# Optimization experiments

Measured on AMD Instinct MI355X. Metric: run time of the kernel, lower is better.

The kernel has to match this reference:

```python
import jax, jax.numpy as jnp
import numpy as np

KERNEL_MUL = 2.0
KERNEL_NUM = 5


def _mmd(source, target):
    n = source.shape[0]
    m = target.shape[0]
    total = jnp.concatenate([source, target], axis=0)  # [n+m, d]
    sq = jnp.sum(total * total, axis=1)  # [n+m]
    l2 = sq[:, None] + sq[None, :] - 2.0 * (total @ total.T)  # [n+m, n+m]
    l2 = jnp.maximum(l2, 0.0)
    n_samples = n + m
    bandwidth = jnp.sum(l2) / (n_samples * n_samples - n_samples)
    bandwidth = bandwidth / (KERNEL_MUL ** (KERNEL_NUM // 2))
    # sum of KERNEL_NUM Gaussian kernels with geometric bandwidths
    kernels = sum(jnp.exp(-l2 / (bandwidth * KERNEL_MUL ** i)) for i in range(KERNEL_NUM))
    b = n  # batch_size = n, as in the torch code
    xx = jnp.sum(kernels[:b, :b]) / (n * n)
    yy = jnp.sum(kernels[b:, b:]) / (m * m)
    xy = jnp.sum(kernels[:b, b:]) / (n * m)
    yx = jnp.sum(kernels[b:, :b]) / (m * n)
    return xx + yy - xy - yx


def setup_inputs() -> dict:
    key = jax.random.key(0)
    k1, k2 = jax.random.split(key)
    source = jax.random.normal(k1, (4096, 256), dtype=jnp.float32)
    target = jax.random.normal(k2, (4096, 256), dtype=jnp.float32)
    return {"source": source, "target": target}


def reference(source, target):
    return _mmd(source, target)
```

## Files before the change

kernel.cpp:

```cpp
#include <hip/hip_runtime.h>
#include <hip/hip_bf16.h>

#define WS_SLOT_OFF   0
#define WS_NEGG_OFF   16640
#define WS_SQPART_OFF 16648
#define WS_CSPART_OFF 17672
#define WS_SQ_OFF     148744
#define WS_G_OFF      181520

#define NROW 8192
#define HALF 4096
#define DIM  256
#define TILE 128
#define NB   64
#define NBLK (NB * (NB + 1) / 2)
#define KC   32
#define NC   (DIM / KC)
#define BUFE (TILE * KC)
#define PREPB 128

typedef short  short8 __attribute__((ext_vector_type(8)));
typedef float  f32x4  __attribute__((ext_vector_type(4)));
typedef float  f32x2  __attribute__((ext_vector_type(2)));
typedef unsigned short us4 __attribute__((ext_vector_type(4)));

static __device__ __forceinline__ unsigned short f2bfbits(float f) {
    __hip_bfloat16 h = __float2bfloat16(f);
    return *reinterpret_cast<unsigned short*>(&h);
}
static __device__ __forceinline__ float bfbits2f(unsigned short u) {
    return __uint_as_float(((unsigned int)u) << 16);
}
static __device__ __forceinline__ void gl_lds16(const void* g, void* l) {
    __builtin_amdgcn_global_load_lds(
        (const __attribute__((address_space(1))) void*)g,
        (__attribute__((address_space(3))) void*)l, 16, 0, 0);
}

__global__ __launch_bounds__(256) void k_prep(const float* __restrict__ src,
                                              const float* __restrict__ tgt,
                                              unsigned short* __restrict__ G,
                                              float* __restrict__ sq,
                                              float* __restrict__ cspart,
                                              double* __restrict__ sqpart) {
    __shared__ float cs_lds[4 * 256];
    __shared__ double sq_lds[4];

    int t = threadIdx.x, wid = t >> 6, lane = t & 63;
    int r0 = blockIdx.x * 64;
    int c4 = lane * 4;

    float cs0 = 0.f, cs1 = 0.f, cs2 = 0.f, cs3 = 0.f;
    double wsq = 0.0;
    for (int i = 0; i < 16; ++i) {
        int row = r0 + wid + i * 4;
        const float* base = (row < HALF) ? (src + (size_t)row * DIM)
                                         : (tgt + (size_t)(row - HALF) * DIM);
        float4 v = *(const float4*)(base + c4);
        unsigned short u0 = f2bfbits(v.x), u1 = f2bfbits(v.y),
                       u2 = f2bfbits(v.z), u3 = f2bfbits(v.w);
        us4 uu = {u0, u1, u2, u3};
        *(us4*)(G + (size_t)row * DIM + c4) = uu;
        float r0f = bfbits2f(u0), r1f = bfbits2f(u1),
              r2f = bfbits2f(u2), r3f = bfbits2f(u3);
        cs0 += r0f; cs1 += r1f; cs2 += r2f; cs3 += r3f;
        float s = r0f * r0f + r1f * r1f + r2f * r2f + r3f * r3f;
        #pragma unroll
        for (int off = 32; off; off >>= 1) s += __shfl_down(s, off);
        if (lane == 0) { sq[row] = s; wsq += (double)s; }
    }
    cs_lds[wid * 256 + c4 + 0] = cs0;
    cs_lds[wid * 256 + c4 + 1] = cs1;
    cs_lds[wid * 256 + c4 + 2] = cs2;
    cs_lds[wid * 256 + c4 + 3] = cs3;
    if (lane == 0) sq_lds[wid] = wsq;
    __syncthreads();
    float s = cs_lds[t] + cs_lds[256 + t] + cs_lds[512 + t] + cs_lds[768 + t];
    cspart[blockIdx.x * 256 + t] = s;
    if (t == 0)
        sqpart[blockIdx.x] = sq_lds[0] + sq_lds[1] + sq_lds[2] + sq_lds[3];
}

__global__ __launch_bounds__(256) void k_bw(const float* __restrict__ cspart,
                                            const double* __restrict__ sqpart,
                                            double* __restrict__ negg) {
    __shared__ double red[256];
    __shared__ double red2[256];
    int t = threadIdx.x;
    double c = 0.0;
    for (int b = 0; b < PREPB; ++b) c += (double)cspart[b * 256 + t];
    double s = (t < PREPB) ? sqpart[t] : 0.0;
    red[t]  = s;
    red2[t] = c * c;
    __syncthreads();
    for (int off = 128; off; off >>= 1) {
        if (t < off) { red[t] += red[t + off]; red2[t] += red2[t + off]; }
        __syncthreads();
    }
    if (t == 0) {
        const double N = (double)NROW;
        double sum_l2 = 2.0 * N * red[0] - 2.0 * red2[0];
        double bw = sum_l2 / (N * N - N);
        bw = bw / 4.0;
        negg[0] = -1.4426950408889634 / (16.0 * bw);
    }
}

__global__ __launch_bounds__(256, 3) void k_mmd(const unsigned short* __restrict__ G,
                                                const float* __restrict__ sq,
                                                const double* __restrict__ negg,
                                                double* __restrict__ slots) {
    __shared__ unsigned short As[3 * BUFE];
    __shared__ unsigned short Bs[3 * BUFE];
    __shared__ double wsum[4];

    int bi = 0, rem = blockIdx.x;
    while (rem >= NB - bi) { rem -= NB - bi; ++bi; }
    int bj = bi + rem;

    int t = threadIdx.x, wid = t >> 6, lane = t & 63;
    int wr = wid >> 1, wc = wid & 1;
    int rl = lane & 15, klane = lane >> 4;

    const unsigned short* Abase = G + (size_t)bi * TILE * DIM;
    const unsigned short* Bbase = G + (size_t)bj * TILE * DIM;

    int lr0 = wid * 32 + (lane >> 2);
    int slog0 = (lane & 3) ^ ((lr0 >> 1) & 3);
    int lr1 = lr0 + 16;
    int slog1 = (lane & 3) ^ ((lr1 >> 1) & 3);
    size_t ga0 = (size_t)lr0 * DIM + slog0 * 8;
    size_t ga1 = (size_t)lr1 * DIM + slog1 * 8;
    int ld0 = (wid * 32) * KC;
    int ld1 = (wid * 32 + 16) * KC;

    int aoff[4], boff[4];
    #pragma unroll
    for (int f = 0; f < 4; ++f) {
        int ra = wr * 64 + f * 16 + rl;
        aoff[f] = ra * KC + ((klane ^ ((ra >> 1) & 3)) * 8);
        int rb = wc * 64 + f * 16 + rl;
        boff[f] = rb * KC + ((klane ^ ((rb >> 1) & 3)) * 8);
    }

    const f32x4 zero4 = {0.f, 0.f, 0.f, 0.f};
    f32x4 acc[4][4];
    #pragma unroll
    for (int i = 0; i < 4; ++i)
        #pragma unroll
        for (int j = 0; j < 4; ++j) acc[i][j] = zero4;

    #define STAGE(kc, b)                                                     \
        do {                                                                 \
            gl_lds16(Abase + ga0 + (kc) * KC, &As[(b) * BUFE + ld0]);        \
            gl_lds16(Bbase + ga0 + (kc) * KC, &Bs[(b) * BUFE + ld0]);        \
            gl_lds16(Abase + ga1 + (kc) * KC, &As[(b) * BUFE + ld1]);        \
            gl_lds16(Bbase + ga1 + (kc) * KC, &Bs[(b) * BUFE + ld1]);        \
        } while (0)

    STAGE(0, 0);
    STAGE(1, 1);

    #pragma unroll
    for (int kc = 0; kc < NC; ++kc) {
        if (kc < NC - 1) { asm volatile("s_waitcnt vmcnt(4)" ::: "memory"); }
        else             { asm volatile("s_waitcnt vmcnt(0)" ::: "memory"); }
        __builtin_amdgcn_s_barrier();
        __builtin_amdgcn_sched_barrier(0);
        if (kc + 2 < NC) STAGE(kc + 2, (kc + 2) % 3);

        const unsigned short* Ab = &As[(kc % 3) * BUFE];
        const unsigned short* Bb = &Bs[(kc % 3) * BUFE];
        short8 af[4], bfv[4];
        #pragma unroll
        for (int f = 0; f < 4; ++f) {
            af[f]  = *(const short8*)&Ab[aoff[f]];
            bfv[f] = *(const short8*)&Bb[boff[f]];
        }
        #pragma unroll
        for (int i = 0; i < 4; ++i)
            #pragma unroll
            for (int j = 0; j < 4; ++j)
                acc[i][j] = __builtin_amdgcn_mfma_f32_16x16x32_bf16(
                    af[i], bfv[j], acc[i][j], 0, 0, 0);
    }
    #undef STAGE

    int gi0 = bi * TILE + wr * 64;
    int gj0 = bj * TILE + wc * 64;
    float ng2 = (float)negg[0];
    float m2g = -2.0f * ng2;
    f32x2 m2g2 = {m2g, m2g};
    int rgrp = lane >> 4;

    float sqb4[4];
    #pragma unroll
    for (int j = 0; j < 4; ++j) sqb4[j] = sq[gj0 + j * 16 + rl] * ng2;

    f32x2 tsv = {0.f, 0.f};
    #pragma unroll
    for (int i = 0; i < 4; ++i) {
        int base = gi0 + i * 16 + rgrp * 4;
        f32x2 sa01 = {sq[base + 0] * ng2, sq[base + 1] * ng2};
        f32x2 sa23 = {sq[base + 2] * ng2, sq[base + 3] * ng2};
        #pragma unroll
        for (int j = 0; j < 4; ++j) {
            f32x2 sb = {sqb4[j], sqb4[j]};
            f32x2 x01 = {acc[i][j][0], acc[i][j][1]};
            f32x2 x23 = {acc[i][j][2], acc[i][j][3]};
            x01 = x01 * m2g2 + (sa01 + sb);
            x23 = x23 * m2g2 + (sa23 + sb);
            f32x2 e01, e23;
            e01.x = exp2f(x01.x); e01.y = exp2f(x01.y);
            e23.x = exp2f(x23.x); e23.y = exp2f(x23.y);
            f32x2 p01 = e01 * e01, q01 = p01 * p01,
                  r01 = q01 * q01, s01 = r01 * r01;
            f32x2 p23 = e23 * e23, q23 = p23 * p23,
                  r23 = q23 * q23, s23 = r23 * r23;
            tsv += ((e01 + p01) + (q01 + r01)) + s01;
            tsv += ((e23 + p23) + (q23 + r23)) + s23;
        }
    }
    float tsum = tsv.x + tsv.y;

    float w = ((bi < 32) == (bj < 32)) ? 1.f : -1.f;
    if (bi != bj) w *= 2.f;
    double dsum = (double)tsum * (double)w;

    #pragma unroll
    for (int off = 32; off; off >>= 1) dsum += __shfl_down(dsum, off);
    if (lane == 0) wsum[wid] = dsum;
    __syncthreads();
    if (t == 0)
        slots[blockIdx.x] = wsum[0] + wsum[1] + wsum[2] + wsum[3];
}

__global__ __launch_bounds__(256) void k_final(const double* __restrict__ slots,
                                               float* __restrict__ out) {
    __shared__ double red[256];
    int t = threadIdx.x;
    double s = 0.0;
    for (int i = t; i < NBLK; i += 256) s += slots[i];
    red[t] = s;
    __syncthreads();
    for (int off = 128; off; off >>= 1) {
        if (t < off) red[t] += red[t + off];
        __syncthreads();
    }
    if (t == 0)
        out[0] = (float)(red[0] / ((double)HALF * (double)HALF));
}

extern "C" void kernel_launch(void* const* d_in, const int* in_sizes, int n_in,
                              void* d_out, int out_size, void* d_ws, size_t ws_size,
                              hipStream_t stream) {
    const float* src = (const float*)d_in[0];
    const float* tgt = (const float*)d_in[1];
    float* out = (float*)d_out;

    double* slots     = (double*)((char*)d_ws + WS_SLOT_OFF);
    double* negg      = (double*)((char*)d_ws + WS_NEGG_OFF);
    double* sqpart    = (double*)((char*)d_ws + WS_SQPART_OFF);
    float*  cspart    = (float*)((char*)d_ws + WS_CSPART_OFF);
    float*  sq        = (float*)((char*)d_ws + WS_SQ_OFF);
    unsigned short* G = (unsigned short*)((char*)d_ws + WS_G_OFF);

    k_prep<<<PREPB, 256, 0, stream>>>(src, tgt, G, sq, cspart, sqpart);
    k_bw<<<1, 256, 0, stream>>>(cspart, sqpart, negg);
    k_mmd<<<NBLK, 256, 0, stream>>>(G, sq, negg, slots);
    k_final<<<1, 256, 0, stream>>>(slots, out);
}
```

Before: 65.38 us.

## Make MMD tile kernel persistent with cross-tile prefetch and swizzled tile order

Replaces the one-block-per-tile-pair grid of 2080 blocks with a persistent grid of 512 blocks, each looping over tile pairs in a strided, swizzled order. A 4-deep LDS ring lets the first K-chunks of the next tile pair load during the tail MMA and exp epilogue of the current one. This aims to hide pipeline fill and launch/tail costs and improve L2 locality, at the cost of lower occupancy (2 blocks per CU instead of 3) and load imbalance, since 2080 pairs do not divide evenly over 512 blocks.

```diff
diff --git a/kernel.cpp b/kernel.cpp
--- a/kernel.cpp
+++ b/kernel.cpp
@@ -2,18 +2,19 @@
 #include <hip/hip_bf16.h>
 
 #define WS_SLOT_OFF   0
-#define WS_NEGG_OFF   16640
-#define WS_SQPART_OFF 16648
-#define WS_CSPART_OFF 17672
-#define WS_SQ_OFF     148744
-#define WS_G_OFF      181520
+#define WS_NEGG_OFF   4096
+#define WS_SQPART_OFF 4104
+#define WS_CSPART_OFF 5128
+#define WS_SQ_OFF     136200
+#define WS_G_OFF      168976
 
 #define NROW 8192
 #define HALF 4096
 #define DIM  256
 #define TILE 128
 #define NB   64
-#define NBLK (NB * (NB + 1) / 2)
+#define NPAIR (NB * (NB + 1) / 2)
+#define GRID_M 512
 #define KC   32
 #define NC   (DIM / KC)
 #define BUFE (TILE * KC)
@@ -106,24 +107,20 @@
     }
 }
 
-__global__ __launch_bounds__(256, 3) void k_mmd(const unsigned short* __restrict__ G,
+__global__ __launch_bounds__(256, 2) void k_mmd(const unsigned short* __restrict__ G,
                                                 const float* __restrict__ sq,
                                                 const double* __restrict__ negg,
                                                 double* __restrict__ slots) {
-    __shared__ unsigned short As[3 * BUFE];
-    __shared__ unsigned short Bs[3 * BUFE];
+    __shared__ unsigned short As[4 * BUFE];
+    __shared__ unsigned short Bs[4 * BUFE];
     __shared__ double wsum[4];
 
-    int bi = 0, rem = blockIdx.x;
-    while (rem >= NB - bi) { rem -= NB - bi; ++bi; }
-    int bj = bi + rem;
+    int bid = blockIdx.x;
+    int swz = (bid & 7) * (GRID_M / 8) + (bid >> 3);
 
     int t = threadIdx.x, wid = t >> 6, lane = t & 63;
     int wr = wid >> 1, wc = wid & 1;
     int rl = lane & 15, klane = lane >> 4;
-
-    const unsigned short* Abase = G + (size_t)bi * TILE * DIM;
-    const unsigned short* Bbase = G + (size_t)bj * TILE * DIM;
 
     int lr0 = wid * 32 + (lane >> 2);
     int slog0 = (lane & 3) ^ ((lr0 >> 1) & 3);
@@ -143,104 +140,136 @@
         boff[f] = rb * KC + ((klane ^ ((rb >> 1) & 3)) * 8);
     }
 
-    const f32x4 zero4 = {0.f, 0.f, 0.f, 0.f};
-    f32x4 acc[4][4];
-    #pragma unroll
-    for (int i = 0; i < 4; ++i)
-        #pragma unroll
-        for (int j = 0; j < 4; ++j) acc[i][j] = zero4;
-
-    #define STAGE(kc, b)                                                     \
-        do {                                                                 \
-            gl_lds16(Abase + ga0 + (kc) * KC, &As[(b) * BUFE + ld0]);        \
-            gl_lds16(Bbase + ga0 + (kc) * KC, &Bs[(b) * BUFE + ld0]);        \
-            gl_lds16(Abase + ga1 + (kc) * KC, &As[(b) * BUFE + ld1]);        \
-            gl_lds16(Bbase + ga1 + (kc) * KC, &Bs[(b) * BUFE + ld1]);        \
-        } while (0)
-
-    STAGE(0, 0);
-    STAGE(1, 1);
-
-    #pragma unroll
-    for (int kc = 0; kc < NC; ++kc) {
-        if (kc < NC - 1) { asm volatile("s_waitcnt vmcnt(4)" ::: "memory"); }
-        else             { asm volatile("s_waitcnt vmcnt(0)" ::: "memory"); }
-        __builtin_amdgcn_s_barrier();
-        __builtin_amdgcn_sched_barrier(0);
-        if (kc + 2 < NC) STAGE(kc + 2, (kc + 2) % 3);
-
-        const unsigned short* Ab = &As[(kc % 3) * BUFE];
-        const unsigned short* Bb = &Bs[(kc % 3) * BUFE];
-        short8 af[4], bfv[4];
-        #pragma unroll
-        for (int f = 0; f < 4; ++f) {
-            af[f]  = *(const short8*)&Ab[aoff[f]];
-            bfv[f] = *(const short8*)&Bb[boff[f]];
-        }
-        #pragma unroll
-        for (int i = 0; i < 4; ++i)
-            #pragma unroll
-            for (int j = 0; j < 4; ++j)
-                acc[i][j] = __builtin_amdgcn_mfma_f32_16x16x32_bf16(
-                    af[i], bfv[j], acc[i][j], 0, 0, 0);
-    }
-    #undef STAGE
-
-    int gi0 = bi * TILE + wr * 64;
-    int gj0 = bj * TILE + wc * 64;
     float ng2 = (float)negg[0];
     float m2g = -2.0f * ng2;
     f32x2 m2g2 = {m2g, m2g};
     int rgrp = lane >> 4;
 
-    float sqb4[4];
+    double bsum = 0.0;
+
+    #define STAGE(Ab_, Bb_, kcc, buf)                                        \
+        do {                                                                 \
+            gl_lds16((Ab_) + ga0 + (kcc) * KC, &As[(buf) * BUFE + ld0]);     \
+            gl_lds16((Bb_) + ga0 + (kcc) * KC, &Bs[(buf) * BUFE + ld0]);     \
+            gl_lds16((Ab_) + ga1 + (kcc) * KC, &As[(buf) * BUFE + ld1]);     \
+            gl_lds16((Bb_) + ga1 + (kcc) * KC, &Bs[(buf) * BUFE + ld1]);     \
+        } while (0)
+
+    int p = swz;
+    int bi = 0, rem = p;
+    while (rem >= NB - bi) { rem -= NB - bi; ++bi; }
+    int bj = bi + rem;
+    const unsigned short* Acur = G + (size_t)bi * TILE * DIM;
+    const unsigned short* Bcur = G + (size_t)bj * TILE * DIM;
+
+    STAGE(Acur, Bcur, 0, 0);
+    STAGE(Acur, Bcur, 1, 1);
+
+    while (true) {
+        int pn = p + GRID_M;
+        bool last = (pn >= NPAIR);
+        const unsigned short* Anxt = Acur;
+        const unsigned short* Bnxt = Bcur;
+        int bin = bi, bjn = bj;
+        if (!last) {
+            int b2 = 0, r2 = pn;
+            while (r2 >= NB - b2) { r2 -= NB - b2; ++b2; }
+            bin = b2; bjn = b2 + r2;
+            Anxt = G + (size_t)bin * TILE * DIM;
+            Bnxt = G + (size_t)bjn * TILE * DIM;
+        }
+
+        const f32x4 zero4 = {0.f, 0.f, 0.f, 0.f};
+        f32x4 acc[4][4];
+        #pragma unroll
+        for (int i = 0; i < 4; ++i)
+            #pragma unroll
+            for (int j = 0; j < 4; ++j) acc[i][j] = zero4;
+
+        #pragma unroll
+        for (int kc = 0; kc < NC; ++kc) {
+            if (kc == NC - 1) {
+                if (last) { asm volatile("s_waitcnt vmcnt(0)" ::: "memory"); }
+                else      { asm volatile("s_waitcnt vmcnt(4)" ::: "memory"); }
+            } else {
+                asm volatile("s_waitcnt vmcnt(4)" ::: "memory");
+            }
+            __builtin_amdgcn_s_barrier();
+            __builtin_amdgcn_sched_barrier(0);
+            if (kc < NC - 2)   { STAGE(Acur, Bcur, kc + 2, (kc + 2) & 3); }
+            else if (!last)    { STAGE(Anxt, Bnxt, kc - 6, (kc + 2) & 3); }
+
+            const unsigned short* Ab = &As[(kc & 3) * BUFE];
+            const unsigned short* Bb = &Bs[(kc & 3) * BUFE];
+            short8 af[4], bfv[4];
+            #pragma unroll
+            for (int f = 0; f < 4; ++f) {
+                af[f]  = *(const short8*)&Ab[aoff[f]];
+                bfv[f] = *(const short8*)&Bb[boff[f]];
+            }
+            #pragma unroll
+            for (int i = 0; i < 4; ++i)
+                #pragma unroll
+                for (int j = 0; j < 4; ++j)
+                    acc[i][j] = __builtin_amdgcn_mfma_f32_16x16x32_bf16(
+                        af[i], bfv[j], acc[i][j], 0, 0, 0);
+        }
+
+        int gi0 = bi * TILE + wr * 64;
+        int gj0 = bj * TILE + wc * 64;
+
+        float sqb4[4];
+        #pragma unroll
+        for (int j = 0; j < 4; ++j) sqb4[j] = sq[gj0 + j * 16 + rl] * ng2;
+
+        f32x2 tsv = {0.f, 0.f};
+        #pragma unroll
+        for (int i = 0; i < 4; ++i) {
+            int base = gi0 + i * 16 + rgrp * 4;
+            f32x2 sa01 = {sq[base + 0] * ng2, sq[base + 1] * ng2};
+            f32x2 sa23 = {sq[base + 2] * ng2, sq[base + 3] * ng2};
+            #pragma unroll
+            for (int j = 0; j < 4; ++j) {
+                f32x2 sb = {sqb4[j], sqb4[j]};
+                f32x2 x01 = {acc[i][j][0], acc[i][j][1]};
+                f32x2 x23 = {acc[i][j][2], acc[i][j][3]};
+                x01 = x01 * m2g2 + (sa01 + sb);
+                x23 = x23 * m2g2 + (sa23 + sb);
+                f32x2 e01, e23;
+                e01.x = exp2f(x01.x); e01.y = exp2f(x01.y);
+                e23.x = exp2f(x23.x); e23.y = exp2f(x23.y);
+                f32x2 p01 = e01 * e01, q01 = p01 * p01,
+                      r01 = q01 * q01, s01 = r01 * r01;
+                f32x2 p23 = e23 * e23, q23 = p23 * p23,
+                      r23 = q23 * q23, s23 = r23 * r23;
+                tsv += ((e01 + p01) + (q01 + r01)) + s01;
+                tsv += ((e23 + p23) + (q23 + r23)) + s23;
+            }
+        }
+        float tsum = tsv.x + tsv.y;
+
+        float w = ((bi < 32) == (bj < 32)) ? 1.f : -1.f;
+        if (bi != bj) w *= 2.f;
+        bsum += (double)(tsum * w);
+
+        if (last) break;
+        p = pn; bi = bin; bj = bjn; Acur = Anxt; Bcur = Bnxt;
+    }
+    #undef STAGE
+
     #pragma unroll
-    for (int j = 0; j < 4; ++j) sqb4[j] = sq[gj0 + j * 16 + rl] * ng2;
-
-    f32x2 tsv = {0.f, 0.f};
-    #pragma unroll
-    for (int i = 0; i < 4; ++i) {
-        int base = gi0 + i * 16 + rgrp * 4;
-        f32x2 sa01 = {sq[base + 0] * ng2, sq[base + 1] * ng2};
-        f32x2 sa23 = {sq[base + 2] * ng2, sq[base + 3] * ng2};
-        #pragma unroll
-        for (int j = 0; j < 4; ++j) {
-            f32x2 sb = {sqb4[j], sqb4[j]};
-            f32x2 x01 = {acc[i][j][0], acc[i][j][1]};
-            f32x2 x23 = {acc[i][j][2], acc[i][j][3]};
-            x01 = x01 * m2g2 + (sa01 + sb);
-            x23 = x23 * m2g2 + (sa23 + sb);
-            f32x2 e01, e23;
-            e01.x = exp2f(x01.x); e01.y = exp2f(x01.y);
-            e23.x = exp2f(x23.x); e23.y = exp2f(x23.y);
-            f32x2 p01 = e01 * e01, q01 = p01 * p01,
-                  r01 = q01 * q01, s01 = r01 * r01;
-            f32x2 p23 = e23 * e23, q23 = p23 * p23,
-                  r23 = q23 * q23, s23 = r23 * r23;
-            tsv += ((e01 + p01) + (q01 + r01)) + s01;
-            tsv += ((e23 + p23) + (q23 + r23)) + s23;
-        }
-    }
-    float tsum = tsv.x + tsv.y;
-
-    float w = ((bi < 32) == (bj < 32)) ? 1.f : -1.f;
-    if (bi != bj) w *= 2.f;
-    double dsum = (double)tsum * (double)w;
-
-    #pragma unroll
-    for (int off = 32; off; off >>= 1) dsum += __shfl_down(dsum, off);
-    if (lane == 0) wsum[wid] = dsum;
+    for (int off = 32; off; off >>= 1) bsum += __shfl_down(bsum, off);
+    if (lane == 0) wsum[wid] = bsum;
     __syncthreads();
     if (t == 0)
-        slots[blockIdx.x] = wsum[0] + wsum[1] + wsum[2] + wsum[3];
+        slots[bid] = wsum[0] + wsum[1] + wsum[2] + wsum[3];
 }
 
 __global__ __launch_bounds__(256) void k_final(const double* __restrict__ slots,
                                                float* __restrict__ out) {
     __shared__ double red[256];
     int t = threadIdx.x;
-    double s = 0.0;
-    for (int i = t; i < NBLK; i += 256) s += slots[i];
+    double s = slots[t] + slots[t + 256];
     red[t] = s;
     __syncthreads();
     for (int off = 128; off; off >>= 1) {
@@ -267,6 +296,6 @@
 
     k_prep<<<PREPB, 256, 0, stream>>>(src, tgt, G, sq, cspart, sqpart);
     k_bw<<<1, 256, 0, stream>>>(cspart, sqpart, negg);
-    k_mmd<<<NBLK, 256, 0, stream>>>(G, sq, negg, slots);
+    k_mmd<<<GRID_M, 256, 0, stream>>>(G, sq, negg, slots);
     k_final<<<1, 256, 0, stream>>>(slots, out);
 }
```

After: 66.67 us. About the same (+2.0%).
